# Kernel tuning notes

Measured on AMD Instinct MI355X. Metric: run time of the kernel, lower is better.

The kernel has to match this reference:

```python
import jax, jax.numpy as jnp
import numpy as np

B, S, E = 2, 2048, 1024
H = 16
DH = E // H
FF = 4096
LN_EPS = 1e-5


def setup_inputs() -> dict:
    key = jax.random.key(0)
    ks = jax.random.split(key, 8)
    s_in = 1.0 / np.sqrt(E)
    s_ff = 1.0 / np.sqrt(FF)
    return {
        "x": jax.random.normal(ks[0], (B, S, E), dtype=jnp.float32),
        "w_qkv": jax.random.normal(ks[1], (E, 3 * E), dtype=jnp.float32) * s_in,
        "b_qkv": jnp.zeros((3 * E,), dtype=jnp.float32),
        "w_proj": jax.random.normal(ks[2], (E, E), dtype=jnp.float32) * s_in,
        "b_proj": jnp.zeros((E,), dtype=jnp.float32),
        "ln_g": jnp.ones((E,), dtype=jnp.float32),
        "ln_b": jnp.zeros((E,), dtype=jnp.float32),
        "w1": jax.random.normal(ks[3], (E, FF), dtype=jnp.float32) * s_in,
        "b1": jnp.zeros((FF,), dtype=jnp.float32),
        "w2": jax.random.normal(ks[4], (FF, E), dtype=jnp.float32) * s_ff,
        "b2": jnp.zeros((E,), dtype=jnp.float32),
    }


def reference(x, w_qkv, b_qkv, w_proj, b_proj, ln_g, ln_b, w1, b1, w2, b2):
    b, s, e = x.shape
    scale = e ** 0.5  # NOTE: original scales by sqrt(embed_dim), not sqrt(head_dim)
    # qkv projection then raw view to [B,3,H,S,Dh] (faithful to torch .view)
    qkv = (x @ w_qkv + b_qkv).reshape(b, 3, H, s, DH)
    q, k, v = qkv[:, 0], qkv[:, 1], qkv[:, 2]  # each [B,H,S,Dh]
    scores = jnp.einsum("bhqd,bhkd->bhqk", q, k) / scale  # [B,H,S,S]
    causal = jnp.tril(jnp.ones((s, s), dtype=bool))
    scores = jnp.where(causal, scores, -jnp.inf)
    attn = jax.nn.softmax(scores, axis=-1)
    h = jnp.einsum("bhqk,bhkd->bhqd", attn, v)  # [B,H,S,Dh]
    h = h.reshape(b, s, e)  # faithful raw view back to [B,S,E]
    h = h @ w_proj + b_proj  # dropout = identity (eval)
    # add & norm
    h = h + x
    mu = jnp.mean(h, axis=-1, keepdims=True)
    var = jnp.var(h, axis=-1, keepdims=True)
    h = (h - mu) * jax.lax.rsqrt(var + LN_EPS) * ln_g + ln_b
    # FFN (dropouts = identity in eval)
    out = jax.nn.relu(h @ w1 + b1) @ w2 + b2
    return out
```

## Files before the change

### kernel.cpp

```cpp
#include <hip/hip_runtime.h>

#define B_ 2
#define S_ 2048
#define E_ 1024
#define H_ 16
#define DH_ 64
#define FF_ 4096

typedef unsigned short bf16_t;
typedef __attribute__((ext_vector_type(8))) short bfrag;
typedef __attribute__((ext_vector_type(4))) float f32x4;
typedef __attribute__((ext_vector_type(16))) float f32x16;
typedef __attribute__((ext_vector_type(4))) unsigned int u32x4;

__device__ __forceinline__ bf16_t f2bf(float x) {
  union { float f; unsigned u; } c; c.f = x;
  return (bf16_t)((c.u + 0x7fffu + ((c.u >> 16) & 1u)) >> 16);
}

__device__ __forceinline__ unsigned pkbf(float lo, float hi) {
  unsigned r;
  asm("v_cvt_pk_bf16_f32 %0, %1, %2" : "=v"(r) : "v"(lo), "v"(hi));
  return r;
}

__device__ __forceinline__ void gload16(const void* g, void* l) {
  __builtin_amdgcn_global_load_lds(
      (const __attribute__((address_space(1))) void*)g,
      (__attribute__((address_space(3))) void*)l, 16, 0, 0);
}

__global__ __launch_bounds__(256) void cvt_kernel(const float* __restrict__ s,
                                                  bf16_t* __restrict__ d) {
  const int i = blockIdx.x * 256 + threadIdx.x;
  const float4 v = ((const float4*)s)[i];
  union { bf16_t u[4]; uint2 uv; } o;
  o.u[0] = f2bf(v.x); o.u[1] = f2bf(v.y); o.u[2] = f2bf(v.z); o.u[3] = f2bf(v.w);
  *(uint2*)(d + (size_t)i * 4) = o.uv;
}

__global__ void transpose_cvt(const float* __restrict__ src, bf16_t* __restrict__ dst,
                              int R, int C) {
  __shared__ float tile[32][33];
  const int c0 = blockIdx.x * 32, r0 = blockIdx.y * 32;
  const int tx = threadIdx.x, ty = threadIdx.y;
#pragma unroll
  for (int i = 0; i < 32; i += 8)
    tile[ty + i][tx] = src[(size_t)(r0 + ty + i) * C + c0 + tx];
  __syncthreads();
#pragma unroll
  for (int i = 0; i < 32; i += 8)
    dst[(size_t)(c0 + ty + i) * R + r0 + tx] = f2bf(tile[tx][ty + i]);
}

__global__ void vtrans_kernel(const bf16_t* __restrict__ qkv, bf16_t* __restrict__ vt) {
  const int bh = blockIdx.z;
  const int b = bh >> 4, h = bh & 15;
  const bf16_t* src = qkv + (size_t)b * S_ * 3 * E_ + (size_t)2 * H_ * S_ * DH_ +
                      (size_t)h * S_ * DH_;
  bf16_t* dst = vt + (size_t)bh * DH_ * S_;
  const int s0 = blockIdx.x * 32, d0 = blockIdx.y * 32;
  __shared__ bf16_t tile[32][33];
  const int tx = threadIdx.x, ty = threadIdx.y;
#pragma unroll
  for (int i = 0; i < 32; i += 8)
    tile[ty + i][tx] = src[(size_t)(s0 + ty + i) * DH_ + d0 + tx];
  __syncthreads();
#pragma unroll
  for (int i = 0; i < 32; i += 8)
    dst[(size_t)(d0 + ty + i) * S_ + s0 + tx] = tile[tx][ty + i];
}


__device__ __forceinline__ void stage_half(const bf16_t* __restrict__ G, int row0,
                                           int kbyte, int Kbytes, bf16_t* ldsreg,
                                           int w, int l) {
#pragma unroll
  for (int j = 0; j < 2; ++j) {
    const int chunk = j * 8 + w;
    const int r = chunk * 8 + (l >> 3);
    const int slot = ((l & 7) ^ (r & 7)) << 4;
    const char* src = (const char*)G + (size_t)(row0 + r) * Kbytes + kbyte + slot;
    gload16(src, (char*)ldsreg + chunk * 1024);
  }
}

__device__ __forceinline__ bfrag ldfrag(const bf16_t* __restrict__ reg, int r, int ks,
                                        int l) {
  int cb = ks * 64 + ((l >> 4) << 4);
  cb ^= (r & 7) << 4;
  return *(const bfrag*)((const char*)reg + r * 128 + cb);
}

template <int MODE>
__global__ __launch_bounds__(512, 2) void gemm8(
    const bf16_t* __restrict__ A, const bf16_t* __restrict__ Bt,
    const float* __restrict__ bias, const float* __restrict__ resid,
    float* __restrict__ outF, bf16_t* __restrict__ outB,
    int M, int N, int K, int ktiles) {
  __shared__ __align__(16) bf16_t lds4[4][256 * 64];
  const int tid = threadIdx.x;
  const int w = tid >> 6, l = tid & 63;
  const int wr = (w >> 2) * 128, wc = (w & 3) * 64;
  const int m0t = blockIdx.y * 256, n0t = blockIdx.x * 256;
  const int Kb = K * 2;
  const int kt0 = (MODE == 4) ? (int)blockIdx.z * ktiles : 0;
  const int ktEnd = kt0 + ktiles;
  if (MODE == 4) outF += (size_t)blockIdx.z * (size_t)M * N;

  stage_half(A, m0t, kt0 * 128, Kb, lds4[0], w, l);
  stage_half(A, m0t + 128, kt0 * 128, Kb, lds4[0] + 8192, w, l);
  stage_half(Bt, n0t, kt0 * 128, Kb, lds4[1], w, l);
  stage_half(Bt, n0t + 128, kt0 * 128, Kb, lds4[1] + 8192, w, l);
  stage_half(Bt, n0t, (kt0 + 1) * 128, Kb, lds4[3], w, l);
  stage_half(Bt, n0t + 128, (kt0 + 1) * 128, Kb, lds4[3] + 8192, w, l);
  asm volatile("s_waitcnt vmcnt(4)" ::: "memory");
  __builtin_amdgcn_s_barrier();

  f32x4 acc[8][4] = {};
  const int fr = l & 15;

  for (int t2 = kt0; t2 < ktEnd; t2 += 2) {
#pragma unroll
    for (int d = 0; d < 2; ++d) {
      const bf16_t* Ar = lds4[d * 2];
      const bf16_t* Br = lds4[d * 2 + 1];
      int sa = t2 + 1 + d; if (sa >= ktEnd) sa = kt0;
      int sb = t2 + 2 + d; if (sb >= ktEnd) sb = kt0;
      bfrag bfr[4][2], afr[2][2];
#pragma unroll
      for (int p = 0; p < 4; ++p) {
        if (p == 0) {
#pragma unroll
          for (int n = 0; n < 4; ++n)
#pragma unroll
            for (int ks = 0; ks < 2; ++ks)
              bfr[n][ks] = ldfrag(Br, wc + n * 16 + fr, ks, l);
        }
#pragma unroll
        for (int mm = 0; mm < 2; ++mm)
#pragma unroll
          for (int ks = 0; ks < 2; ++ks)
            afr[mm][ks] = ldfrag(Ar, wr + p * 32 + mm * 16 + fr, ks, l);
        if (p == 0)      stage_half(A, m0t, sa * 128, Kb, lds4[(d ^ 1) * 2], w, l);
        else if (p == 1) stage_half(A, m0t + 128, sa * 128, Kb, lds4[(d ^ 1) * 2] + 8192, w, l);
        else if (p == 2) stage_half(Bt, n0t, sb * 128, Kb, lds4[d * 2 + 1], w, l);
        else             stage_half(Bt, n0t + 128, sb * 128, Kb, lds4[d * 2 + 1] + 8192, w, l);
        __builtin_amdgcn_s_barrier();
        asm volatile("s_waitcnt lgkmcnt(0)" ::: "memory");
        __builtin_amdgcn_sched_barrier(0);
        __builtin_amdgcn_s_setprio(1);
#pragma unroll
        for (int mm = 0; mm < 2; ++mm)
#pragma unroll
          for (int n = 0; n < 4; ++n)
#pragma unroll
            for (int ks = 0; ks < 2; ++ks)
              acc[p * 2 + mm][n] = __builtin_amdgcn_mfma_f32_16x16x32_bf16(
                  afr[mm][ks], bfr[n][ks], acc[p * 2 + mm][n], 0, 0, 0);
        __builtin_amdgcn_s_setprio(0);
        if (p == 3) asm volatile("s_waitcnt vmcnt(4)" ::: "memory");
        __builtin_amdgcn_s_barrier();
      }
    }
  }

  const int cr = (l >> 4) * 4, cc = l & 15;
#pragma unroll
  for (int n = 0; n < 4; ++n) {
    const int gc = n0t + wc + n * 16 + cc;
    const float bn = (MODE == 4) ? 0.f : bias[gc];
#pragma unroll
    for (int m = 0; m < 8; ++m) {
      const int gr0 = m0t + wr + m * 16 + cr;
#pragma unroll
      for (int j = 0; j < 4; ++j) {
        float v = acc[m][n][j] + bn;
        const size_t idx = (size_t)(gr0 + j) * N + gc;
        if (MODE == 1) v += resid[idx];
        if (MODE == 2) v = fmaxf(v, 0.f);
        if (MODE == 0 || MODE == 2) outB[idx] = f2bf(v);
        else outF[idx] = v;
      }
    }
  }
}

__global__ __launch_bounds__(256) void red2_kernel(const float* __restrict__ p,
                                                   const float* __restrict__ bias,
                                                   float* __restrict__ out) {
  const size_t i = ((size_t)blockIdx.x * 256 + threadIdx.x) * 4;
  const size_t PS = (size_t)4096 * 1024;
  const float4 a = *(const float4*)(p + i);
  const float4 b = *(const float4*)(p + PS + i);
  const float4 bb = *(const float4*)(bias + (i & 1023));
  float4 o;
  o.x = a.x + b.x + bb.x;
  o.y = a.y + b.y + bb.y;
  o.z = a.z + b.z + bb.z;
  o.w = a.w + b.w + bb.w;
  *(float4*)(out + i) = o;
}

#define C1_ 0.0450842213f

template <bool MASK>
__device__ __forceinline__ void attn_step(const bf16_t* __restrict__ Kp,
                                          const bf16_t* __restrict__ Vt,
                                          int kv0, const bfrag* qf, f32x16& o0,
                                          f32x16& o1, float& m, float& lsum,
                                          int lq32, int hi) {
  bfrag kf[4];
#pragma unroll
  for (int c = 0; c < 4; ++c)
    kf[c] = *(const bfrag*)&Kp[(size_t)(kv0 + lq32) * DH_ + c * 16 + hi * 8];
  f32x16 st;
#pragma unroll
  for (int j = 0; j < 16; ++j) st[j] = 0.f;
#pragma unroll
  for (int c = 0; c < 4; ++c)
    st = __builtin_amdgcn_mfma_f32_32x32x16_bf16(kf[c], qf[c], st, 0, 0, 0);
  if (MASK) {
#pragma unroll
    for (int r = 0; r < 16; ++r) {
      const int kvloc = (r & 3) + 8 * (r >> 2) + 4 * hi;
      st[r] = (kvloc <= lq32) ? st[r] : -3.0e38f;
    }
  }
  float pm = st[0];
#pragma unroll
  for (int j = 1; j < 16; ++j) pm = fmaxf(pm, st[j]);
  pm = fmaxf(pm, __shfl_xor(pm, 32));
  if (!__all(pm <= m + 128.0f)) {
    const float mn = fmaxf(m, pm);
    const float corr = exp2f((m - mn) * C1_);
    m = mn;
    lsum *= corr;
#pragma unroll
    for (int j = 0; j < 16; ++j) { o0[j] *= corr; o1[j] *= corr; }
  }
  const float mc = m * C1_;
  float p[16];
  float ps = 0.f;
#pragma unroll
  for (int j = 0; j < 16; ++j) {
    p[j] = exp2f(__builtin_fmaf(st[j], C1_, -mc));
    ps += p[j];
  }
  ps += __shfl_xor(ps, 32);
  lsum += ps;
  unsigned wv[8], ov[8];
#pragma unroll
  for (int j = 0; j < 8; ++j) wv[j] = pkbf(p[2 * j], p[2 * j + 1]);
#pragma unroll
  for (int j = 0; j < 8; ++j) ov[j] = (unsigned)__shfl_xor((int)wv[j], 32);
  union { unsigned u[4]; bfrag f; } f0, f1;
  f0.u[0] = hi ? ov[2] : wv[0];
  f0.u[1] = hi ? ov[3] : wv[1];
  f0.u[2] = hi ? wv[2] : ov[0];
  f0.u[3] = hi ? wv[3] : ov[1];
  f1.u[0] = hi ? ov[6] : wv[4];
  f1.u[1] = hi ? ov[7] : wv[5];
  f1.u[2] = hi ? wv[6] : ov[4];
  f1.u[3] = hi ? wv[7] : ov[5];
#pragma unroll
  for (int t = 0; t < 2; ++t) {
    const bf16_t* vr = &Vt[(size_t)(t * 32 + lq32) * S_ + kv0 + hi * 8];
    bfrag v0 = *(const bfrag*)vr;
    bfrag v1 = *(const bfrag*)(vr + 16);
    f32x16& ot = t ? o1 : o0;
    ot = __builtin_amdgcn_mfma_f32_32x32x16_bf16(v0, f0.f, ot, 0, 0, 0);
    ot = __builtin_amdgcn_mfma_f32_32x32x16_bf16(v1, f1.f, ot, 0, 0, 0);
  }
}

__global__ __launch_bounds__(256, 6) void attn_kernel(const bf16_t* __restrict__ qkv,
                                                      const bf16_t* __restrict__ vt,
                                                      bf16_t* __restrict__ outp) {
  __shared__ float obuf[2][32][66];
  __shared__ float ml[4][2][32];
  __shared__ float lst[32];
  const int tid = threadIdx.x;
  const int w = tid >> 6, l = tid & 63;
  const int lq32 = l & 31, hi = l >> 5;
  const int lid = blockIdx.x;
  const int xcd = lid & 7;
  const int idx = lid >> 3;
  const int by = xcd * 4 + (idx >> 6);
  const int qblk = 63 - (idx & 63);
  const int b = by >> 4, h = by & 15;
  const size_t bbase = (size_t)b * S_ * 3 * E_;
  const bf16_t* Q = qkv + bbase + (size_t)h * S_ * DH_;
  const bf16_t* Kp = Q + (size_t)H_ * S_ * DH_;
  const bf16_t* Vt = vt + (size_t)by * DH_ * S_;
  bf16_t* Og = outp + (size_t)by * S_ * DH_;
  const int q0 = qblk * 32;

  bfrag qf[4];
#pragma unroll
  for (int c = 0; c < 4; ++c)
    qf[c] = *(const bfrag*)&Q[(size_t)(q0 + lq32) * DH_ + c * 16 + hi * 8];

  f32x16 o0, o1;
#pragma unroll
  for (int j = 0; j < 16; ++j) { o0[j] = 0.f; o1[j] = 0.f; }
  float m = -3.0e38f, lsum = 0.f;

  const int nfull = qblk;
  for (int s = w; s < nfull; s += 4)
    attn_step<false>(Kp, Vt, s * 32, qf, o0, o1, m, lsum, lq32, hi);
  if ((nfull & 3) == w)
    attn_step<true>(Kp, Vt, q0, qf, o0, o1, m, lsum, lq32, hi);

  if (hi == 0) { ml[w][0][lq32] = m; ml[w][1][lq32] = lsum; }
  __syncthreads();
  const float m0 = ml[0][0][lq32], m1 = ml[1][0][lq32];
  const float m2 = ml[2][0][lq32], m3 = ml[3][0][lq32];
  const float mstar = fmaxf(fmaxf(m0, m1), fmaxf(m2, m3));
  const float lstar = ml[0][1][lq32] * exp2f((m0 - mstar) * C1_) +
                      ml[1][1][lq32] * exp2f((m1 - mstar) * C1_) +
                      ml[2][1][lq32] * exp2f((m2 - mstar) * C1_) +
                      ml[3][1][lq32] * exp2f((m3 - mstar) * C1_);
  if (w == 0 && hi == 0) lst[lq32] = lstar;
  const float myscale = exp2f((m - mstar) * C1_);
#pragma unroll
  for (int j = 0; j < 16; ++j) { o0[j] *= myscale; o1[j] *= myscale; }
  if (w < 2) {
#pragma unroll
    for (int t = 0; t < 2; ++t) {
      const f32x16& oo = t ? o1 : o0;
#pragma unroll
      for (int g = 0; g < 4; ++g) {
        const int d = t * 32 + g * 8 + hi * 4;
        *(float2*)&obuf[w][lq32][d] = make_float2(oo[g * 4 + 0], oo[g * 4 + 1]);
        *(float2*)&obuf[w][lq32][d + 2] = make_float2(oo[g * 4 + 2], oo[g * 4 + 3]);
      }
    }
  }
  __syncthreads();
  if (w >= 2) {
#pragma unroll
    for (int t = 0; t < 2; ++t) {
      const f32x16& oo = t ? o1 : o0;
#pragma unroll
      for (int g = 0; g < 4; ++g) {
        const int d = t * 32 + g * 8 + hi * 4;
        float2 a = *(const float2*)&obuf[w - 2][lq32][d];
        float2 c = *(const float2*)&obuf[w - 2][lq32][d + 2];
        a.x += oo[g * 4 + 0]; a.y += oo[g * 4 + 1];
        c.x += oo[g * 4 + 2]; c.y += oo[g * 4 + 3];
        *(float2*)&obuf[w - 2][lq32][d] = a;
        *(float2*)&obuf[w - 2][lq32][d + 2] = c;
      }
    }
  }
  __syncthreads();
  const int q = tid >> 3, dc = (tid & 7) * 8;
  const float linv = 1.0f / lst[q];
  union { unsigned u[4]; u32x4 v; } pk;
#pragma unroll
  for (int g = 0; g < 4; ++g) {
    float2 a = *(const float2*)&obuf[0][q][dc + g * 2];
    float2 c = *(const float2*)&obuf[1][q][dc + g * 2];
    pk.u[g] = pkbf((a.x + c.x) * linv, (a.y + c.y) * linv);
  }
  *(u32x4*)&Og[(size_t)(q0 + q) * DH_ + dc] = pk.v;
}

__device__ __forceinline__ void ln_core(float4 v, int t, const float* g,
                                        const float* be, bf16_t* orow) {
  float s = v.x + v.y + v.z + v.w;
  float q = v.x * v.x + v.y * v.y + v.z * v.z + v.w * v.w;
#pragma unroll
  for (int d = 1; d < 64; d <<= 1) { s += __shfl_xor(s, d); q += __shfl_xor(q, d); }
  __shared__ float red[8];
  const int w = t >> 6;
  if ((t & 63) == 0) { red[w] = s; red[4 + w] = q; }
  __syncthreads();
  s = red[0] + red[1] + red[2] + red[3];
  q = red[4] + red[5] + red[6] + red[7];
  const float mu = s * (1.f / E_);
  const float var = q * (1.f / E_) - mu * mu;
  const float rs = rsqrtf(var + 1e-5f);
  const float4 gg = ((const float4*)g)[t];
  const float4 bb = ((const float4*)be)[t];
  union { bf16_t u[4]; uint2 uv; } o;
  o.u[0] = f2bf((v.x - mu) * rs * gg.x + bb.x);
  o.u[1] = f2bf((v.y - mu) * rs * gg.y + bb.y);
  o.u[2] = f2bf((v.z - mu) * rs * gg.z + bb.z);
  o.u[3] = f2bf((v.w - mu) * rs * gg.w + bb.w);
  *(uint2*)(orow + t * 4) = o.uv;
}

__global__ __launch_bounds__(256) void ln_kernel(const float* __restrict__ hin,
                                                 const float* __restrict__ g,
                                                 const float* __restrict__ be,
                                                 bf16_t* __restrict__ outp) {
  const int row = blockIdx.x, t = threadIdx.x;
  const float4 v = ((const float4*)(hin + (size_t)row * E_))[t];
  ln_core(v, t, g, be, outp + (size_t)row * E_);
}

__global__ __launch_bounds__(256) void ln2_kernel(const float* __restrict__ p,
                                                  const float* __restrict__ x,
                                                  const float* __restrict__ bproj,
                                                  const float* __restrict__ g,
                                                  const float* __restrict__ be,
                                                  bf16_t* __restrict__ outp) {
  const int row = blockIdx.x, t = threadIdx.x;
  const size_t PS = (size_t)4096 * 1024;
  const size_t off = (size_t)row * E_ + t * 4;
  const float4 a = *(const float4*)(p + off);
  const float4 b = *(const float4*)(p + PS + off);
  const float4 xr = *(const float4*)(x + off);
  const float4 bp = *(const float4*)(bproj + t * 4);
  float4 v;
  v.x = a.x + b.x + xr.x + bp.x;
  v.y = a.y + b.y + xr.y + bp.y;
  v.z = a.z + b.z + xr.z + bp.z;
  v.w = a.w + b.w + xr.w + bp.w;
  ln_core(v, t, g, be, outp + (size_t)row * E_);
}

extern "C" void kernel_launch(void* const* d_in, const int* in_sizes, int n_in,
                              void* d_out, int out_size, void* d_ws, size_t ws_size,
                              hipStream_t stream) {
  (void)in_sizes; (void)n_in; (void)out_size;
  const float* x      = (const float*)d_in[0];
  const float* w_qkv  = (const float*)d_in[1];
  const float* b_qkv  = (const float*)d_in[2];
  const float* w_proj = (const float*)d_in[3];
  const float* b_proj = (const float*)d_in[4];
  const float* ln_g   = (const float*)d_in[5];
  const float* ln_b   = (const float*)d_in[6];
  const float* w1     = (const float*)d_in[7];
  const float* b1     = (const float*)d_in[8];
  const float* w2     = (const float*)d_in[9];
  const float* b2     = (const float*)d_in[10];
  float* out = (float*)d_out;
  char* ws = (char*)d_ws;
  const size_t MB = (size_t)1 << 20;
  bf16_t* w2T    = (bf16_t*)(ws + 0 * MB);
  bf16_t* w1T    = (bf16_t*)(ws + 8 * MB);
  bf16_t* vtb    = (bf16_t*)(ws + 16 * MB);
  bf16_t* lnb    = (bf16_t*)(ws + 16 * MB);
  bf16_t* wqkvT  = (bf16_t*)(ws + 24 * MB);
  bf16_t* wprojT = (bf16_t*)(ws + 30 * MB);
  bf16_t* attnb  = (bf16_t*)(ws + 32 * MB);
  bf16_t* xb     = (bf16_t*)(ws + 40 * MB);
  bf16_t* qkvb   = (bf16_t*)(ws + 48 * MB);
  float*  pparts = (float*)(ws + 48 * MB);
  float*  hbuf   = (float*)(ws + 48 * MB);
  bf16_t* ffn1b  = (bf16_t*)(ws + 48 * MB);
  float*  fparts = (float*)(ws + 80 * MB);
  const bool splitk = ws_size >= 112 * MB;

  dim3 tb(32, 8);
  cvt_kernel<<<4096, 256, 0, stream>>>(x, xb);
  transpose_cvt<<<dim3(3072 / 32, 1024 / 32), tb, 0, stream>>>(w_qkv, wqkvT, 1024, 3072);
  transpose_cvt<<<dim3(1024 / 32, 1024 / 32), tb, 0, stream>>>(w_proj, wprojT, 1024, 1024);
  transpose_cvt<<<dim3(4096 / 32, 1024 / 32), tb, 0, stream>>>(w1, w1T, 1024, 4096);
  transpose_cvt<<<dim3(1024 / 32, 4096 / 32), tb, 0, stream>>>(w2, w2T, 4096, 1024);

  gemm8<0><<<dim3(12, 16), 512, 0, stream>>>(xb, wqkvT, b_qkv, nullptr, nullptr, qkvb,
                                             4096, 3072, 1024, 16);

  vtrans_kernel<<<dim3(S_ / 32, 2, 32), tb, 0, stream>>>(qkvb, vtb);
  attn_kernel<<<dim3(2048), 256, 0, stream>>>(qkvb, vtb, attnb);

  if (splitk) {
    gemm8<4><<<dim3(4, 16, 2), 512, 0, stream>>>(attnb, wprojT, nullptr, nullptr,
                                                 pparts, nullptr, 4096, 1024, 1024, 8);
    ln2_kernel<<<4096, 256, 0, stream>>>(pparts, x, b_proj, ln_g, ln_b, lnb);
    gemm8<2><<<dim3(16, 16), 512, 0, stream>>>(lnb, w1T, b1, nullptr, nullptr, ffn1b,
                                               4096, 4096, 1024, 16);
    gemm8<4><<<dim3(4, 16, 2), 512, 0, stream>>>(ffn1b, w2T, nullptr, nullptr, fparts,
                                                 nullptr, 4096, 1024, 4096, 32);
    red2_kernel<<<4096, 256, 0, stream>>>(fparts, b2, out);
  } else {
    gemm8<1><<<dim3(4, 16), 512, 0, stream>>>(attnb, wprojT, b_proj, x, hbuf, nullptr,
                                              4096, 1024, 1024, 16);
    ln_kernel<<<4096, 256, 0, stream>>>(hbuf, ln_g, ln_b, lnb);
    gemm8<2><<<dim3(16, 16), 512, 0, stream>>>(lnb, w1T, b1, nullptr, nullptr, ffn1b,
                                               4096, 4096, 1024, 16);
    gemm8<3><<<dim3(4, 16), 512, 0, stream>>>(ffn1b, w2T, b2, nullptr, out, nullptr,
                                              4096, 1024, 4096, 64);
  }
}
```

Before: 291.3 us.

## Restructure attention: one query tile per wave, 64-wide KV steps with K prefetch

The attention kernel now gives each wave its own 32-query tile inside a 128-query block, instead of splitting one 32-query tile's KV range across four waves. That removes the cross-wave softmax merge and its shared-memory reductions and barriers. The inner loop processes 64 keys per step, double-buffers K fragments in registers, and uses tree reductions for row max and sum. Grid size drops to 512 blocks and launch bounds are relaxed, so register pressure and occupancy change and per-block causal work is less balanced.

```diff
diff --git a/kernel.cpp b/kernel.cpp
--- a/kernel.cpp
+++ b/kernel.cpp
@@ -204,6 +204,101 @@
 
 #define C1_ 0.0450842213f
 
+struct kvK { bfrag a[4]; bfrag b[4]; };
+
+__device__ __forceinline__ void loadK(kvK& s, const bf16_t* __restrict__ Kp, int kv0,
+                                      int lq32, int hi) {
+#pragma unroll
+  for (int c = 0; c < 4; ++c)
+    s.a[c] = *(const bfrag*)&Kp[(size_t)(kv0 + lq32) * DH_ + c * 16 + hi * 8];
+#pragma unroll
+  for (int c = 0; c < 4; ++c)
+    s.b[c] = *(const bfrag*)&Kp[(size_t)(kv0 + 32 + lq32) * DH_ + c * 16 + hi * 8];
+}
+
+__device__ __forceinline__ void compute64(const kvK& s, const bf16_t* __restrict__ Vt,
+                                          int kv0, const bfrag* qf, f32x16& o0,
+                                          f32x16& o1, float& m, float& lsum,
+                                          int lq32, int hi) {
+  bfrag vA[4], vB[4];
+#pragma unroll
+  for (int t = 0; t < 2; ++t) {
+    const bf16_t* vr = &Vt[(size_t)(t * 32 + lq32) * S_ + kv0 + hi * 8];
+    vA[2 * t] = *(const bfrag*)vr;
+    vA[2 * t + 1] = *(const bfrag*)(vr + 16);
+    vB[2 * t] = *(const bfrag*)(vr + 32);
+    vB[2 * t + 1] = *(const bfrag*)(vr + 48);
+  }
+  f32x16 stA, stB;
+#pragma unroll
+  for (int j = 0; j < 16; ++j) { stA[j] = 0.f; stB[j] = 0.f; }
+#pragma unroll
+  for (int c = 0; c < 4; ++c)
+    stA = __builtin_amdgcn_mfma_f32_32x32x16_bf16(s.a[c], qf[c], stA, 0, 0, 0);
+#pragma unroll
+  for (int c = 0; c < 4; ++c)
+    stB = __builtin_amdgcn_mfma_f32_32x32x16_bf16(s.b[c], qf[c], stB, 0, 0, 0);
+  float mx[16];
+#pragma unroll
+  for (int j = 0; j < 16; ++j) mx[j] = fmaxf(stA[j], stB[j]);
+#pragma unroll
+  for (int st = 8; st >= 1; st >>= 1)
+#pragma unroll
+    for (int j = 0; j < st; ++j) mx[j] = fmaxf(mx[j], mx[j + st]);
+  float pm = fmaxf(mx[0], __shfl_xor(mx[0], 32));
+  if (!__all(pm <= m + 128.0f)) {
+    const float mn = fmaxf(m, pm);
+    const float corr = exp2f((m - mn) * C1_);
+    m = mn;
+    lsum *= corr;
+#pragma unroll
+    for (int j = 0; j < 16; ++j) { o0[j] *= corr; o1[j] *= corr; }
+  }
+  const float mc = m * C1_;
+  float pA[16], pB[16];
+#pragma unroll
+  for (int j = 0; j < 16; ++j) {
+    pA[j] = exp2f(__builtin_fmaf(stA[j], C1_, -mc));
+    pB[j] = exp2f(__builtin_fmaf(stB[j], C1_, -mc));
+  }
+  float sm[16];
+#pragma unroll
+  for (int j = 0; j < 16; ++j) sm[j] = pA[j] + pB[j];
+#pragma unroll
+  for (int st = 8; st >= 1; st >>= 1)
+#pragma unroll
+    for (int j = 0; j < st; ++j) sm[j] += sm[j + st];
+  lsum += sm[0] + __shfl_xor(sm[0], 32);
+  unsigned wvA[8], ovA[8], wvB[8], ovB[8];
+#pragma unroll
+  for (int j = 0; j < 8; ++j) {
+    wvA[j] = pkbf(pA[2 * j], pA[2 * j + 1]);
+    wvB[j] = pkbf(pB[2 * j], pB[2 * j + 1]);
+  }
+#pragma unroll
+  for (int j = 0; j < 8; ++j) {
+    ovA[j] = (unsigned)__shfl_xor((int)wvA[j], 32);
+    ovB[j] = (unsigned)__shfl_xor((int)wvB[j], 32);
+  }
+  union { unsigned u[4]; bfrag f; } f0A, f1A, f0B, f1B;
+  f0A.u[0] = hi ? ovA[2] : wvA[0];  f0A.u[1] = hi ? ovA[3] : wvA[1];
+  f0A.u[2] = hi ? wvA[2] : ovA[0];  f0A.u[3] = hi ? wvA[3] : ovA[1];
+  f1A.u[0] = hi ? ovA[6] : wvA[4];  f1A.u[1] = hi ? ovA[7] : wvA[5];
+  f1A.u[2] = hi ? wvA[6] : ovA[4];  f1A.u[3] = hi ? wvA[7] : ovA[5];
+  f0B.u[0] = hi ? ovB[2] : wvB[0];  f0B.u[1] = hi ? ovB[3] : wvB[1];
+  f0B.u[2] = hi ? wvB[2] : ovB[0];  f0B.u[3] = hi ? wvB[3] : ovB[1];
+  f1B.u[0] = hi ? ovB[6] : wvB[4];  f1B.u[1] = hi ? ovB[7] : wvB[5];
+  f1B.u[2] = hi ? wvB[6] : ovB[4];  f1B.u[3] = hi ? wvB[7] : ovB[5];
+  o0 = __builtin_amdgcn_mfma_f32_32x32x16_bf16(vA[0], f0A.f, o0, 0, 0, 0);
+  o1 = __builtin_amdgcn_mfma_f32_32x32x16_bf16(vA[2], f0A.f, o1, 0, 0, 0);
+  o0 = __builtin_amdgcn_mfma_f32_32x32x16_bf16(vA[1], f1A.f, o0, 0, 0, 0);
+  o1 = __builtin_amdgcn_mfma_f32_32x32x16_bf16(vA[3], f1A.f, o1, 0, 0, 0);
+  o0 = __builtin_amdgcn_mfma_f32_32x32x16_bf16(vB[0], f0B.f, o0, 0, 0, 0);
+  o1 = __builtin_amdgcn_mfma_f32_32x32x16_bf16(vB[2], f0B.f, o1, 0, 0, 0);
+  o0 = __builtin_amdgcn_mfma_f32_32x32x16_bf16(vB[1], f1B.f, o0, 0, 0, 0);
+  o1 = __builtin_amdgcn_mfma_f32_32x32x16_bf16(vB[3], f1B.f, o1, 0, 0, 0);
+}
+
 template <bool MASK>
 __device__ __forceinline__ void attn_step(const bf16_t* __restrict__ Kp,
                                           const bf16_t* __restrict__ Vt,
@@ -227,10 +322,14 @@
       st[r] = (kvloc <= lq32) ? st[r] : -3.0e38f;
     }
   }
-  float pm = st[0];
-#pragma unroll
-  for (int j = 1; j < 16; ++j) pm = fmaxf(pm, st[j]);
-  pm = fmaxf(pm, __shfl_xor(pm, 32));
+  float mx[8];
+#pragma unroll
+  for (int j = 0; j < 8; ++j) mx[j] = fmaxf(st[j], st[j + 8]);
+#pragma unroll
+  for (int stp = 4; stp >= 1; stp >>= 1)
+#pragma unroll
+    for (int j = 0; j < stp; ++j) mx[j] = fmaxf(mx[j], mx[j + stp]);
+  float pm = fmaxf(mx[0], __shfl_xor(mx[0], 32));
   if (!__all(pm <= m + 128.0f)) {
     const float mn = fmaxf(m, pm);
     const float corr = exp2f((m - mn) * C1_);
@@ -241,28 +340,26 @@
   }
   const float mc = m * C1_;
   float p[16];
-  float ps = 0.f;
-#pragma unroll
-  for (int j = 0; j < 16; ++j) {
-    p[j] = exp2f(__builtin_fmaf(st[j], C1_, -mc));
-    ps += p[j];
-  }
-  ps += __shfl_xor(ps, 32);
-  lsum += ps;
+#pragma unroll
+  for (int j = 0; j < 16; ++j) p[j] = exp2f(__builtin_fmaf(st[j], C1_, -mc));
+  float sm[8];
+#pragma unroll
+  for (int j = 0; j < 8; ++j) sm[j] = p[j] + p[j + 8];
+#pragma unroll
+  for (int stp = 4; stp >= 1; stp >>= 1)
+#pragma unroll
+    for (int j = 0; j < stp; ++j) sm[j] += sm[j + stp];
+  lsum += sm[0] + __shfl_xor(sm[0], 32);
   unsigned wv[8], ov[8];
 #pragma unroll
   for (int j = 0; j < 8; ++j) wv[j] = pkbf(p[2 * j], p[2 * j + 1]);
 #pragma unroll
   for (int j = 0; j < 8; ++j) ov[j] = (unsigned)__shfl_xor((int)wv[j], 32);
   union { unsigned u[4]; bfrag f; } f0, f1;
-  f0.u[0] = hi ? ov[2] : wv[0];
-  f0.u[1] = hi ? ov[3] : wv[1];
-  f0.u[2] = hi ? wv[2] : ov[0];
-  f0.u[3] = hi ? wv[3] : ov[1];
-  f1.u[0] = hi ? ov[6] : wv[4];
-  f1.u[1] = hi ? ov[7] : wv[5];
-  f1.u[2] = hi ? wv[6] : ov[4];
-  f1.u[3] = hi ? wv[7] : ov[5];
+  f0.u[0] = hi ? ov[2] : wv[0];  f0.u[1] = hi ? ov[3] : wv[1];
+  f0.u[2] = hi ? wv[2] : ov[0];  f0.u[3] = hi ? wv[3] : ov[1];
+  f1.u[0] = hi ? ov[6] : wv[4];  f1.u[1] = hi ? ov[7] : wv[5];
+  f1.u[2] = hi ? wv[6] : ov[4];  f1.u[3] = hi ? wv[7] : ov[5];
 #pragma unroll
   for (int t = 0; t < 2; ++t) {
     const bf16_t* vr = &Vt[(size_t)(t * 32 + lq32) * S_ + kv0 + hi * 8];
@@ -274,97 +371,74 @@
   }
 }
 
-__global__ __launch_bounds__(256, 6) void attn_kernel(const bf16_t* __restrict__ qkv,
+__global__ __launch_bounds__(256, 2) void attn_kernel(const bf16_t* __restrict__ qkv,
                                                       const bf16_t* __restrict__ vt,
                                                       bf16_t* __restrict__ outp) {
-  __shared__ float obuf[2][32][66];
-  __shared__ float ml[4][2][32];
-  __shared__ float lst[32];
+  __shared__ unsigned short otl[4][32 * 72];
   const int tid = threadIdx.x;
   const int w = tid >> 6, l = tid & 63;
   const int lq32 = l & 31, hi = l >> 5;
   const int lid = blockIdx.x;
   const int xcd = lid & 7;
   const int idx = lid >> 3;
-  const int by = xcd * 4 + (idx >> 6);
-  const int qblk = 63 - (idx & 63);
+  const int by = xcd * 4 + (idx >> 4);
+  const int qg = 15 - (idx & 15);
   const int b = by >> 4, h = by & 15;
   const size_t bbase = (size_t)b * S_ * 3 * E_;
   const bf16_t* Q = qkv + bbase + (size_t)h * S_ * DH_;
   const bf16_t* Kp = Q + (size_t)H_ * S_ * DH_;
   const bf16_t* Vt = vt + (size_t)by * DH_ * S_;
   bf16_t* Og = outp + (size_t)by * S_ * DH_;
-  const int q0 = qblk * 32;
+  const int q0w = qg * 128 + w * 32;
 
   bfrag qf[4];
 #pragma unroll
   for (int c = 0; c < 4; ++c)
-    qf[c] = *(const bfrag*)&Q[(size_t)(q0 + lq32) * DH_ + c * 16 + hi * 8];
+    qf[c] = *(const bfrag*)&Q[(size_t)(q0w + lq32) * DH_ + c * 16 + hi * 8];
 
   f32x16 o0, o1;
 #pragma unroll
   for (int j = 0; j < 16; ++j) { o0[j] = 0.f; o1[j] = 0.f; }
   float m = -3.0e38f, lsum = 0.f;
 
-  const int nfull = qblk;
-  for (int s = w; s < nfull; s += 4)
-    attn_step<false>(Kp, Vt, s * 32, qf, o0, o1, m, lsum, lq32, hi);
-  if ((nfull & 3) == w)
-    attn_step<true>(Kp, Vt, q0, qf, o0, o1, m, lsum, lq32, hi);
-
-  if (hi == 0) { ml[w][0][lq32] = m; ml[w][1][lq32] = lsum; }
-  __syncthreads();
-  const float m0 = ml[0][0][lq32], m1 = ml[1][0][lq32];
-  const float m2 = ml[2][0][lq32], m3 = ml[3][0][lq32];
-  const float mstar = fmaxf(fmaxf(m0, m1), fmaxf(m2, m3));
-  const float lstar = ml[0][1][lq32] * exp2f((m0 - mstar) * C1_) +
-                      ml[1][1][lq32] * exp2f((m1 - mstar) * C1_) +
-                      ml[2][1][lq32] * exp2f((m2 - mstar) * C1_) +
-                      ml[3][1][lq32] * exp2f((m3 - mstar) * C1_);
-  if (w == 0 && hi == 0) lst[lq32] = lstar;
-  const float myscale = exp2f((m - mstar) * C1_);
-#pragma unroll
-  for (int j = 0; j < 16; ++j) { o0[j] *= myscale; o1[j] *= myscale; }
-  if (w < 2) {
-#pragma unroll
-    for (int t = 0; t < 2; ++t) {
-      const f32x16& oo = t ? o1 : o0;
-#pragma unroll
-      for (int g = 0; g < 4; ++g) {
-        const int d = t * 32 + g * 8 + hi * 4;
-        *(float2*)&obuf[w][lq32][d] = make_float2(oo[g * 4 + 0], oo[g * 4 + 1]);
-        *(float2*)&obuf[w][lq32][d + 2] = make_float2(oo[g * 4 + 2], oo[g * 4 + 3]);
-      }
+  const int n64 = q0w >> 6;
+  kvK s0, s1;
+  if (n64 > 0) loadK(s0, Kp, 0, lq32, hi);
+  for (int it = 0; it < n64; ++it) {
+    const int nxt = (it + 1) * 64;
+    if ((it & 1) == 0) {
+      if (it + 1 < n64) loadK(s1, Kp, nxt, lq32, hi);
+      compute64(s0, Vt, it * 64, qf, o0, o1, m, lsum, lq32, hi);
+    } else {
+      if (it + 1 < n64) loadK(s0, Kp, nxt, lq32, hi);
+      compute64(s1, Vt, it * 64, qf, o0, o1, m, lsum, lq32, hi);
     }
   }
-  __syncthreads();
-  if (w >= 2) {
-#pragma unroll
-    for (int t = 0; t < 2; ++t) {
-      const f32x16& oo = t ? o1 : o0;
-#pragma unroll
-      for (int g = 0; g < 4; ++g) {
-        const int d = t * 32 + g * 8 + hi * 4;
-        float2 a = *(const float2*)&obuf[w - 2][lq32][d];
-        float2 c = *(const float2*)&obuf[w - 2][lq32][d + 2];
-        a.x += oo[g * 4 + 0]; a.y += oo[g * 4 + 1];
-        c.x += oo[g * 4 + 2]; c.y += oo[g * 4 + 3];
-        *(float2*)&obuf[w - 2][lq32][d] = a;
-        *(float2*)&obuf[w - 2][lq32][d + 2] = c;
-      }
+  if (q0w & 32)
+    attn_step<false>(Kp, Vt, q0w - 32, qf, o0, o1, m, lsum, lq32, hi);
+  attn_step<true>(Kp, Vt, q0w, qf, o0, o1, m, lsum, lq32, hi);
+
+  const float linv = 1.0f / lsum;
+  unsigned short* otw = otl[w];
+#pragma unroll
+  for (int t = 0; t < 2; ++t) {
+    const f32x16& oo = t ? o1 : o0;
+#pragma unroll
+    for (int g = 0; g < 4; ++g) {
+      const int d = t * 32 + g * 8 + hi * 4;
+      uint2 v;
+      v.x = pkbf(oo[g * 4 + 0] * linv, oo[g * 4 + 1] * linv);
+      v.y = pkbf(oo[g * 4 + 2] * linv, oo[g * 4 + 3] * linv);
+      *(uint2*)&otw[lq32 * 72 + d] = v;
     }
   }
-  __syncthreads();
-  const int q = tid >> 3, dc = (tid & 7) * 8;
-  const float linv = 1.0f / lst[q];
-  union { unsigned u[4]; u32x4 v; } pk;
-#pragma unroll
-  for (int g = 0; g < 4; ++g) {
-    float2 a = *(const float2*)&obuf[0][q][dc + g * 2];
-    float2 c = *(const float2*)&obuf[1][q][dc + g * 2];
-    pk.u[g] = pkbf((a.x + c.x) * linv, (a.y + c.y) * linv);
-  }
-  *(u32x4*)&Og[(size_t)(q0 + q) * DH_ + dc] = pk.v;
+  asm volatile("s_waitcnt lgkmcnt(0)" ::: "memory");
+  const int q = l >> 1, hh = l & 1;
+#pragma unroll
+  for (int i = 0; i < 4; ++i) {
+    u32x4 v = *(const u32x4*)&otw[q * 72 + hh * 32 + i * 8];
+    *(u32x4*)&Og[(size_t)(q0w + q) * DH_ + hh * 32 + i * 8] = v;
+  }
 }
 
 __device__ __forceinline__ void ln_core(float4 v, int t, const float* g,
@@ -466,7 +540,7 @@
                                              4096, 3072, 1024, 16);
 
   vtrans_kernel<<<dim3(S_ / 32, 2, 32), tb, 0, stream>>>(qkvb, vtb);
-  attn_kernel<<<dim3(2048), 256, 0, stream>>>(qkvb, vtb, attnb);
+  attn_kernel<<<dim3(512), 256, 0, stream>>>(qkvb, vtb, attnb);
 
   if (splitk) {
     gemm8<4><<<dim3(4, 16, 2), 512, 0, stream>>>(attnb, wprojT, nullptr, nullptr,
```

After: 317.5 us. 1.09x slower.

## Give each attention wave its own query tile with K prefetch, dropping cross-wave merge

Applied to the files above, without the earlier changes.

The attention kernel now assigns each of the four waves a separate 32-row query tile inside a 128-row block, rather than splitting one tile's KV range across waves. This removes the shared-memory softmax merge and its barriers. The grid shrinks from 2048 to 512 blocks, with a balanced pairing of light and heavy causal tiles. K fragments are prefetched one step ahead, V loads are issued before the QK MFMAs, and the max and sum reductions use trees. The cost is fewer blocks, a lower occupancy hint, more registers, and per-wave causal imbalance inside a block.

```diff
diff --git a/kernel.cpp b/kernel.cpp
--- a/kernel.cpp
+++ b/kernel.cpp
@@ -204,22 +204,37 @@
 
 #define C1_ 0.0450842213f
 
+struct kf4 { bfrag k[4]; };
+
+__device__ __forceinline__ kf4 loadK32(const bf16_t* __restrict__ Kp, int kv0,
+                                       int lq32, int hi) {
+  kf4 r;
+#pragma unroll
+  for (int c = 0; c < 4; ++c)
+    r.k[c] = *(const bfrag*)&Kp[(size_t)(kv0 + lq32) * DH_ + c * 16 + hi * 8];
+  return r;
+}
+
 template <bool MASK>
-__device__ __forceinline__ void attn_step(const bf16_t* __restrict__ Kp,
-                                          const bf16_t* __restrict__ Vt,
+__device__ __forceinline__ void compute32(const kf4& s, const bf16_t* __restrict__ Vt,
                                           int kv0, const bfrag* qf, f32x16& o0,
                                           f32x16& o1, float& m, float& lsum,
                                           int lq32, int hi) {
-  bfrag kf[4];
+  bfrag v00, v01, v10, v11;
+  {
+    const bf16_t* vr = &Vt[(size_t)lq32 * S_ + kv0 + hi * 8];
+    v00 = *(const bfrag*)vr;
+    v01 = *(const bfrag*)(vr + 16);
+    const bf16_t* vr2 = &Vt[(size_t)(32 + lq32) * S_ + kv0 + hi * 8];
+    v10 = *(const bfrag*)vr2;
+    v11 = *(const bfrag*)(vr2 + 16);
+  }
+  f32x16 st;
+#pragma unroll
+  for (int j = 0; j < 16; ++j) st[j] = 0.f;
 #pragma unroll
   for (int c = 0; c < 4; ++c)
-    kf[c] = *(const bfrag*)&Kp[(size_t)(kv0 + lq32) * DH_ + c * 16 + hi * 8];
-  f32x16 st;
-#pragma unroll
-  for (int j = 0; j < 16; ++j) st[j] = 0.f;
-#pragma unroll
-  for (int c = 0; c < 4; ++c)
-    st = __builtin_amdgcn_mfma_f32_32x32x16_bf16(kf[c], qf[c], st, 0, 0, 0);
+    st = __builtin_amdgcn_mfma_f32_32x32x16_bf16(s.k[c], qf[c], st, 0, 0, 0);
   if (MASK) {
 #pragma unroll
     for (int r = 0; r < 16; ++r) {
@@ -227,10 +242,14 @@
       st[r] = (kvloc <= lq32) ? st[r] : -3.0e38f;
     }
   }
-  float pm = st[0];
-#pragma unroll
-  for (int j = 1; j < 16; ++j) pm = fmaxf(pm, st[j]);
-  pm = fmaxf(pm, __shfl_xor(pm, 32));
+  float mx[8];
+#pragma unroll
+  for (int j = 0; j < 8; ++j) mx[j] = fmaxf(st[j], st[j + 8]);
+#pragma unroll
+  for (int stp = 4; stp >= 1; stp >>= 1)
+#pragma unroll
+    for (int j = 0; j < stp; ++j) mx[j] = fmaxf(mx[j], mx[j + stp]);
+  float pm = fmaxf(mx[0], __shfl_xor(mx[0], 32));
   if (!__all(pm <= m + 128.0f)) {
     const float mn = fmaxf(m, pm);
     const float corr = exp2f((m - mn) * C1_);
@@ -241,130 +260,93 @@
   }
   const float mc = m * C1_;
   float p[16];
-  float ps = 0.f;
-#pragma unroll
-  for (int j = 0; j < 16; ++j) {
-    p[j] = exp2f(__builtin_fmaf(st[j], C1_, -mc));
-    ps += p[j];
-  }
-  ps += __shfl_xor(ps, 32);
-  lsum += ps;
+#pragma unroll
+  for (int j = 0; j < 16; ++j) p[j] = exp2f(__builtin_fmaf(st[j], C1_, -mc));
+  float sm[8];
+#pragma unroll
+  for (int j = 0; j < 8; ++j) sm[j] = p[j] + p[j + 8];
+#pragma unroll
+  for (int stp = 4; stp >= 1; stp >>= 1)
+#pragma unroll
+    for (int j = 0; j < stp; ++j) sm[j] += sm[j + stp];
+  lsum += sm[0] + __shfl_xor(sm[0], 32);
   unsigned wv[8], ov[8];
 #pragma unroll
   for (int j = 0; j < 8; ++j) wv[j] = pkbf(p[2 * j], p[2 * j + 1]);
 #pragma unroll
   for (int j = 0; j < 8; ++j) ov[j] = (unsigned)__shfl_xor((int)wv[j], 32);
   union { unsigned u[4]; bfrag f; } f0, f1;
-  f0.u[0] = hi ? ov[2] : wv[0];
-  f0.u[1] = hi ? ov[3] : wv[1];
-  f0.u[2] = hi ? wv[2] : ov[0];
-  f0.u[3] = hi ? wv[3] : ov[1];
-  f1.u[0] = hi ? ov[6] : wv[4];
-  f1.u[1] = hi ? ov[7] : wv[5];
-  f1.u[2] = hi ? wv[6] : ov[4];
-  f1.u[3] = hi ? wv[7] : ov[5];
-#pragma unroll
-  for (int t = 0; t < 2; ++t) {
-    const bf16_t* vr = &Vt[(size_t)(t * 32 + lq32) * S_ + kv0 + hi * 8];
-    bfrag v0 = *(const bfrag*)vr;
-    bfrag v1 = *(const bfrag*)(vr + 16);
-    f32x16& ot = t ? o1 : o0;
-    ot = __builtin_amdgcn_mfma_f32_32x32x16_bf16(v0, f0.f, ot, 0, 0, 0);
-    ot = __builtin_amdgcn_mfma_f32_32x32x16_bf16(v1, f1.f, ot, 0, 0, 0);
-  }
-}
-
-__global__ __launch_bounds__(256, 6) void attn_kernel(const bf16_t* __restrict__ qkv,
+  f0.u[0] = hi ? ov[2] : wv[0];  f0.u[1] = hi ? ov[3] : wv[1];
+  f0.u[2] = hi ? wv[2] : ov[0];  f0.u[3] = hi ? wv[3] : ov[1];
+  f1.u[0] = hi ? ov[6] : wv[4];  f1.u[1] = hi ? ov[7] : wv[5];
+  f1.u[2] = hi ? wv[6] : ov[4];  f1.u[3] = hi ? wv[7] : ov[5];
+  o0 = __builtin_amdgcn_mfma_f32_32x32x16_bf16(v00, f0.f, o0, 0, 0, 0);
+  o1 = __builtin_amdgcn_mfma_f32_32x32x16_bf16(v10, f0.f, o1, 0, 0, 0);
+  o0 = __builtin_amdgcn_mfma_f32_32x32x16_bf16(v01, f1.f, o0, 0, 0, 0);
+  o1 = __builtin_amdgcn_mfma_f32_32x32x16_bf16(v11, f1.f, o1, 0, 0, 0);
+}
+
+__global__ __launch_bounds__(256, 2) void attn_kernel(const bf16_t* __restrict__ qkv,
                                                       const bf16_t* __restrict__ vt,
                                                       bf16_t* __restrict__ outp) {
-  __shared__ float obuf[2][32][66];
-  __shared__ float ml[4][2][32];
-  __shared__ float lst[32];
+  __shared__ unsigned short otl[4][32 * 72];
   const int tid = threadIdx.x;
   const int w = tid >> 6, l = tid & 63;
   const int lq32 = l & 31, hi = l >> 5;
   const int lid = blockIdx.x;
   const int xcd = lid & 7;
-  const int idx = lid >> 3;
-  const int by = xcd * 4 + (idx >> 6);
-  const int qblk = 63 - (idx & 63);
+  const int i = lid >> 3;
+  const int by = xcd * 4 + (i & 3);
+  const int qi = i >> 2;
+  const int qt = (qi & 1) ? (15 - (qi >> 1)) : (qi >> 1);
   const int b = by >> 4, h = by & 15;
   const size_t bbase = (size_t)b * S_ * 3 * E_;
   const bf16_t* Q = qkv + bbase + (size_t)h * S_ * DH_;
   const bf16_t* Kp = Q + (size_t)H_ * S_ * DH_;
   const bf16_t* Vt = vt + (size_t)by * DH_ * S_;
   bf16_t* Og = outp + (size_t)by * S_ * DH_;
-  const int q0 = qblk * 32;
+  const int q0w = qt * 128 + w * 32;
 
   bfrag qf[4];
 #pragma unroll
   for (int c = 0; c < 4; ++c)
-    qf[c] = *(const bfrag*)&Q[(size_t)(q0 + lq32) * DH_ + c * 16 + hi * 8];
+    qf[c] = *(const bfrag*)&Q[(size_t)(q0w + lq32) * DH_ + c * 16 + hi * 8];
 
   f32x16 o0, o1;
 #pragma unroll
   for (int j = 0; j < 16; ++j) { o0[j] = 0.f; o1[j] = 0.f; }
   float m = -3.0e38f, lsum = 0.f;
 
-  const int nfull = qblk;
-  for (int s = w; s < nfull; s += 4)
-    attn_step<false>(Kp, Vt, s * 32, qf, o0, o1, m, lsum, lq32, hi);
-  if ((nfull & 3) == w)
-    attn_step<true>(Kp, Vt, q0, qf, o0, o1, m, lsum, lq32, hi);
-
-  if (hi == 0) { ml[w][0][lq32] = m; ml[w][1][lq32] = lsum; }
-  __syncthreads();
-  const float m0 = ml[0][0][lq32], m1 = ml[1][0][lq32];
-  const float m2 = ml[2][0][lq32], m3 = ml[3][0][lq32];
-  const float mstar = fmaxf(fmaxf(m0, m1), fmaxf(m2, m3));
-  const float lstar = ml[0][1][lq32] * exp2f((m0 - mstar) * C1_) +
-                      ml[1][1][lq32] * exp2f((m1 - mstar) * C1_) +
-                      ml[2][1][lq32] * exp2f((m2 - mstar) * C1_) +
-                      ml[3][1][lq32] * exp2f((m3 - mstar) * C1_);
-  if (w == 0 && hi == 0) lst[lq32] = lstar;
-  const float myscale = exp2f((m - mstar) * C1_);
-#pragma unroll
-  for (int j = 0; j < 16; ++j) { o0[j] *= myscale; o1[j] *= myscale; }
-  if (w < 2) {
-#pragma unroll
-    for (int t = 0; t < 2; ++t) {
-      const f32x16& oo = t ? o1 : o0;
-#pragma unroll
-      for (int g = 0; g < 4; ++g) {
-        const int d = t * 32 + g * 8 + hi * 4;
-        *(float2*)&obuf[w][lq32][d] = make_float2(oo[g * 4 + 0], oo[g * 4 + 1]);
-        *(float2*)&obuf[w][lq32][d + 2] = make_float2(oo[g * 4 + 2], oo[g * 4 + 3]);
-      }
+  const int nsteps = q0w >> 5;
+  kf4 kcur = loadK32(Kp, 0, lq32, hi);
+  for (int s = 0; s < nsteps; ++s) {
+    kf4 knxt = loadK32(Kp, (s + 1) * 32, lq32, hi);
+    compute32<false>(kcur, Vt, s * 32, qf, o0, o1, m, lsum, lq32, hi);
+    kcur = knxt;
+  }
+  compute32<true>(kcur, Vt, q0w, qf, o0, o1, m, lsum, lq32, hi);
+
+  const float linv = 1.0f / lsum;
+  unsigned short* otw = otl[w];
+#pragma unroll
+  for (int t = 0; t < 2; ++t) {
+    const f32x16& oo = t ? o1 : o0;
+#pragma unroll
+    for (int g = 0; g < 4; ++g) {
+      const int d = t * 32 + g * 8 + hi * 4;
+      uint2 v;
+      v.x = pkbf(oo[g * 4 + 0] * linv, oo[g * 4 + 1] * linv);
+      v.y = pkbf(oo[g * 4 + 2] * linv, oo[g * 4 + 3] * linv);
+      *(uint2*)&otw[lq32 * 72 + d] = v;
     }
   }
-  __syncthreads();
-  if (w >= 2) {
-#pragma unroll
-    for (int t = 0; t < 2; ++t) {
-      const f32x16& oo = t ? o1 : o0;
-#pragma unroll
-      for (int g = 0; g < 4; ++g) {
-        const int d = t * 32 + g * 8 + hi * 4;
-        float2 a = *(const float2*)&obuf[w - 2][lq32][d];
-        float2 c = *(const float2*)&obuf[w - 2][lq32][d + 2];
-        a.x += oo[g * 4 + 0]; a.y += oo[g * 4 + 1];
-        c.x += oo[g * 4 + 2]; c.y += oo[g * 4 + 3];
-        *(float2*)&obuf[w - 2][lq32][d] = a;
-        *(float2*)&obuf[w - 2][lq32][d + 2] = c;
-      }
-    }
-  }
-  __syncthreads();
-  const int q = tid >> 3, dc = (tid & 7) * 8;
-  const float linv = 1.0f / lst[q];
-  union { unsigned u[4]; u32x4 v; } pk;
-#pragma unroll
-  for (int g = 0; g < 4; ++g) {
-    float2 a = *(const float2*)&obuf[0][q][dc + g * 2];
-    float2 c = *(const float2*)&obuf[1][q][dc + g * 2];
-    pk.u[g] = pkbf((a.x + c.x) * linv, (a.y + c.y) * linv);
-  }
-  *(u32x4*)&Og[(size_t)(q0 + q) * DH_ + dc] = pk.v;
+  asm volatile("s_waitcnt lgkmcnt(0)" ::: "memory");
+  const int q = l >> 1, hh = l & 1;
+#pragma unroll
+  for (int ii = 0; ii < 4; ++ii) {
+    u32x4 v = *(const u32x4*)&otw[q * 72 + hh * 32 + ii * 8];
+    *(u32x4*)&Og[(size_t)(q0w + q) * DH_ + hh * 32 + ii * 8] = v;
+  }
 }
 
 __device__ __forceinline__ void ln_core(float4 v, int t, const float* g,
@@ -466,7 +448,7 @@
                                              4096, 3072, 1024, 16);
 
   vtrans_kernel<<<dim3(S_ / 32, 2, 32), tb, 0, stream>>>(qkvb, vtb);
-  attn_kernel<<<dim3(2048), 256, 0, stream>>>(qkvb, vtb, attnb);
+  attn_kernel<<<dim3(512), 256, 0, stream>>>(qkvb, vtb, attnb);
 
   if (splitk) {
     gemm8<4><<<dim3(4, 16, 2), 512, 0, stream>>>(attnb, wprojT, nullptr, nullptr,
```

Result: no change. 292.3 us (+0.4%).
